# Optimization experiments

Measured on AMD Instinct MI355X. Metric: run time of the kernel, lower is better.

The kernel has to match this reference:

```python
import jax, jax.numpy as jnp
import numpy as np

B, L, DIM = 4, 2048, 512
H, D = 8, 64
SCALE = D ** -0.5
NEG = -10000.0


def setup_inputs() -> dict:
    key = jax.random.key(0)
    ks = jax.random.split(key, 5)
    std = 1.0 / np.sqrt(DIM)
    return {
        "x": jax.random.normal(ks[0], (B, L, DIM), dtype=jnp.float32),
        "wq": jax.random.normal(ks[1], (H * D, DIM), dtype=jnp.float32) * std,
        "wk": jax.random.normal(ks[2], (H * D, DIM), dtype=jnp.float32) * std,
        "wv": jax.random.normal(ks[3], (H * D, DIM), dtype=jnp.float32) * std,
        "wo": jax.random.normal(ks[4], (DIM, H * D), dtype=jnp.float32) * std,
    }


def reference(x, wq, wk, wv, wo):
    b, l, _ = x.shape
    # projections (torch Linear: y = x @ W.T), split heads -> [b,h,l,d]
    q = (x @ wq.T).reshape(b, l, H, D).transpose(0, 2, 1, 3)
    k = (x @ wk.T).reshape(b, l, H, D).transpose(0, 2, 1, 3)
    v = (x @ wv.T).reshape(b, l, H, D).transpose(0, 2, 1, 3)
    scores = jnp.einsum("bhld,bhsd->bhls", q, k) * SCALE
    scores = jnp.nan_to_num(scores, nan=0.0, posinf=10000.0, neginf=NEG)
    diag = jnp.eye(l, dtype=bool)[None, None]  # [1,1,l,l]
    scores = jnp.where(diag, NEG, scores)
    attn = jax.nn.softmax(scores, axis=-1)
    attn = jnp.where(diag, 0.0, attn)
    attn = jnp.nan_to_num(attn, nan=0.0, posinf=0.0, neginf=0.0)
    out = jnp.einsum("bhls,bhsd->bhld", attn, v)
    out = out.transpose(0, 2, 1, 3).reshape(b, l, H * D)
    return out @ wo.T
```

## Files before the change

### kernel.cpp

```cpp
#include <hip/hip_runtime.h>
#include <hip/hip_bf16.h>


#define Bsz 4
#define Lsz 2048
#define DIMsz 512
#define Hsz 8
#define Dsz 64

typedef _Float16 f16;
typedef __attribute__((ext_vector_type(8))) _Float16 f16x8;
typedef __attribute__((ext_vector_type(4))) _Float16 f16x4;
typedef __attribute__((ext_vector_type(2))) __fp16 fp16x2;
typedef __attribute__((ext_vector_type(4))) float f32x4;
typedef __attribute__((ext_vector_type(16))) float f32x16;
typedef unsigned int u32;
typedef __attribute__((ext_vector_type(2))) unsigned int u32x2;

#if __has_builtin(__builtin_amdgcn_exp2f)
#define EXP2(x) __builtin_amdgcn_exp2f(x)
#else
#define EXP2(x) __expf(0.6931471805599453f * (x))
#endif

__device__ __forceinline__ u32 pack2(float a, float b) {
#if __has_builtin(__builtin_amdgcn_cvt_pkrtz)
    fp16x2 h = __builtin_amdgcn_cvt_pkrtz(a, b);
    return __builtin_bit_cast(u32, h);
#else
    fp16x2 h; h.x = (__fp16)a; h.y = (__fp16)b;
    return __builtin_bit_cast(u32, h);
#endif
}

#if __has_builtin(__builtin_amdgcn_permlane32_swap)
__device__ __forceinline__ void plswap(u32& a, u32& b) {
    u32x2 r = __builtin_amdgcn_permlane32_swap(a, b, false, false);
    a = r.x; b = r.y;
}
#else
__device__ __forceinline__ void plswap(u32& a, u32& b) {
    u32 sa = (u32)__shfl_xor((int)a, 32);
    u32 sb = (u32)__shfl_xor((int)b, 32);
    bool hi = (threadIdx.x & 32) != 0;
    u32 na = hi ? sb : a;
    u32 nb = hi ? b : sa;
    a = na; b = nb;
}
#endif

__device__ __forceinline__ void gl2lds16(const void* g, void* l) {
    __builtin_amdgcn_global_load_lds(
        (const __attribute__((address_space(1))) u32*)g,
        (__attribute__((address_space(3))) u32*)l, 16, 0, 0);
}

__global__ __launch_bounds__(256) void pack_f16(
    const float* __restrict__ x, const float* __restrict__ wq,
    const float* __restrict__ wk, const float* __restrict__ wv,
    const float* __restrict__ wo,
    f16* __restrict__ xh, f16* __restrict__ w3h, f16* __restrict__ woh)
{
    int bx = blockIdx.x, seg, blk;
    if (bx < 4096) { seg = 0; blk = bx; }
    else { seg = 1 + ((bx - 4096) >> 8); blk = (bx - 4096) & 255; }
    const float* s; f16* d; float sc = 1.0f;
    switch (seg) {
        case 0: s = x;  d = xh;            break;
        case 1: s = wq; d = w3h;           sc = 0.18033688011112042f; break;
        case 2: s = wk; d = w3h + 262144;  break;
        case 3: s = wv; d = w3h + 524288;  break;
        default: s = wo; d = woh;          break;
    }
    int i = (blk * 256 + threadIdx.x) * 4;
    float4 v = *(const float4*)(s + i);
    f16x4 o;
    o.x = (f16)(v.x * sc); o.y = (f16)(v.y * sc);
    o.z = (f16)(v.z * sc); o.w = (f16)(v.w * sc);
    *(f16x4*)(d + i) = o;
}

__global__ __launch_bounds__(256) void gemm_qkv_f16(
    const f16* __restrict__ A, const f16* __restrict__ B,
    f16* __restrict__ qh, f16* __restrict__ kh, f16* __restrict__ vth)
{
    __shared__ __align__(16) char smem[32768];
    f16* Ash = (f16*)smem;
    f16* Bsh = (f16*)(smem + 16384);

    const int tid = threadIdx.x;
    const int w = tid >> 6, lane = tid & 63;
    const int quad = lane >> 4, low = lane & 15;
    const int wm = w >> 1, wn = w & 1;
    const int m0 = blockIdx.y * 128, n0 = blockIdx.x * 128;

    f32x4 acc[4][4];
    #pragma unroll
    for (int i = 0; i < 4; i++)
        #pragma unroll
        for (int j = 0; j < 4; j++) acc[i][j] = (f32x4){0.f, 0.f, 0.f, 0.f};

    #pragma unroll 1
    for (int k0 = 0; k0 < DIMsz; k0 += 64) {
        __syncthreads();
        #pragma unroll
        for (int j = 0; j < 4; j++) {
            int t = j * 256 + tid;
            int r = t >> 3, g = t & 7;
            int gc = (g ^ (r & 7)) * 8;
            char* lb = (char*)Ash + (j * 256 + w * 64) * 16;
            gl2lds16(A + (size_t)(m0 + r) * DIMsz + k0 + gc, lb);
            char* lb2 = (char*)Bsh + (j * 256 + w * 64) * 16;
            gl2lds16(B + (size_t)(n0 + r) * DIMsz + k0 + gc, lb2);
        }
        __syncthreads();

        #pragma unroll
        for (int ks2 = 0; ks2 < 2; ks2++) {
            f16x8 af[4], bf[4];
            #pragma unroll
            for (int mt = 0; mt < 4; mt++) {
                int ar = wm * 64 + mt * 16 + low;
                int c = ks2 * 4 + quad;
                af[mt] = *(const f16x8*)&Ash[ar * 64 + ((c ^ (ar & 7)) << 3)];
            }
            #pragma unroll
            for (int nt = 0; nt < 4; nt++) {
                int br = wn * 64 + nt * 16 + low;
                int c = ks2 * 4 + quad;
                bf[nt] = *(const f16x8*)&Bsh[br * 64 + ((c ^ (br & 7)) << 3)];
            }
            #pragma unroll
            for (int mt = 0; mt < 4; mt++)
                #pragma unroll
                for (int nt = 0; nt < 4; nt++)
                    acc[mt][nt] = __builtin_amdgcn_mfma_f32_16x16x32_f16(
                        af[mt], bf[nt], acc[mt][nt], 0, 0, 0);
        }
    }

    const int proj = n0 >> 9;
    if (proj < 2) {
        f16* dst = (proj == 0) ? qh : kh;
        #pragma unroll
        for (int nt = 0; nt < 4; nt++) {
            int n = n0 + wn * 64 + nt * 16 + low;
            int c = n & 511, h = c >> 6, d = c & 63;
            #pragma unroll
            for (int mt = 0; mt < 4; mt++)
                #pragma unroll
                for (int r = 0; r < 4; r++) {
                    int m = m0 + wm * 64 + mt * 16 + quad * 4 + r;
                    int b_ = m >> 11, l = m & (Lsz - 1);
                    size_t bh = (size_t)(b_ * Hsz + h);
                    dst[(bh * Lsz + l) * Dsz + d] = (f16)acc[mt][nt][r];
                }
        }
    } else {
        const int hb = (n0 & 511) >> 6;
        f16* Tv = (f16*)smem;
        const int b_ = m0 >> 11, l0 = m0 & (Lsz - 1);
        #pragma unroll 1
        for (int hs = 0; hs < 2; hs++) {
            __syncthreads();
            if (wn == hs) {
                #pragma unroll
                for (int nt = 0; nt < 4; nt++) {
                    int d = nt * 16 + low;
                    #pragma unroll
                    for (int mt = 0; mt < 4; mt++)
                        #pragma unroll
                        for (int r = 0; r < 4; r++) {
                            int l = wm * 64 + mt * 16 + quad * 4 + r;
                            Tv[d * 136 + l] = (f16)acc[mt][nt][r];
                        }
                }
            }
            __syncthreads();
            int d = tid >> 2, seg = tid & 3;
            size_t bh = (size_t)(b_ * Hsz + hb + hs);
            f16* dstp = vth + (bh * 64 + d) * (size_t)Lsz + l0 + seg * 32;
            const f16* srcp = Tv + d * 136 + seg * 32;
            #pragma unroll
            for (int j = 0; j < 4; j++)
                *(f16x8*)(dstp + j * 8) = *(const f16x8*)(srcp + j * 8);
        }
    }
}

__global__ __launch_bounds__(256) void attn_mfma(
    const f16* __restrict__ q, const f16* __restrict__ k,
    const f16* __restrict__ vt, f16* __restrict__ ctx)
{
    __shared__ __align__(16) char smem[32768];
    __shared__ float Ls[2][32];

    f16* Ks = (f16*)smem;
    f16* Vs = (f16*)(smem + 16384);

    const int tid = threadIdx.x;
    const int w = tid >> 6, lane = tid & 63;
    const int col = lane & 31;
    const int h = lane >> 5;
    const int bh = blockIdx.x;
    const int qb = blockIdx.y;
    const int grp = w >> 1;
    const int kw = w & 1;
    const int q0w = qb * 64 + grp * 32;
    const size_t kvb = (size_t)bh * Lsz;

    f16x8 qf[4];
    #pragma unroll
    for (int s = 0; s < 4; s++)
        qf[s] = *(const f16x8*)(q + (kvb + q0w + col) * Dsz + s * 16 + h * 8);

    f32x16 acc[2];
    #pragma unroll
    for (int dt = 0; dt < 2; dt++)
        #pragma unroll
        for (int i = 0; i < 16; i++) acc[dt][i] = 0.f;
    float lsum = 0.f;

    #pragma unroll 1
    for (int s0 = 0; s0 < Lsz; s0 += 128) {
        __syncthreads();
        #pragma unroll
        for (int i = 0; i < 4; i++) {
            int idx = i * 256 + tid;
            int rk = idx >> 3, gk = idx & 7;
            int rv = idx >> 4, gv = idx & 15;
            char* kl = (char*)Ks + (i * 256 + w * 64) * 16;
            char* vl = (char*)Vs + (i * 256 + w * 64) * 16;
            gl2lds16(k + (kvb + s0 + rk) * Dsz + ((gk ^ (rk & 7)) << 3), kl);
            gl2lds16(vt + ((size_t)bh * Dsz + rv) * Lsz + s0 + ((gv ^ (rv & 15)) << 3), vl);
        }
        __syncthreads();

        #pragma unroll
        for (int sc = 0; sc < 2; sc++) {
            f32x16 st;
            #pragma unroll
            for (int i = 0; i < 16; i++) st[i] = 0.f;
            const int rk = sc * 64 + kw * 32 + col;
            #pragma unroll
            for (int s = 0; s < 4; s++) {
                f16x8 kf = *(const f16x8*)(Ks + rk * 64 +
                               (((s * 2 + h) ^ (rk & 7)) << 3));
                st = __builtin_amdgcn_mfma_f32_32x32x16_f16(kf, qf[s], st, 0, 0, 0);
            }

            float pv[16];
            #pragma unroll
            for (int i = 0; i < 16; i++) pv[i] = EXP2(st[i]);
            if (s0 + sc * 64 == qb * 64 && kw == grp) {
                #pragma unroll
                for (int i = 0; i < 16; i++) {
                    int row = (i & 3) + 8 * (i >> 2) + 4 * h;
                    pv[i] = (row == col) ? 0.f : pv[i];
                }
            }
            #pragma unroll
            for (int i = 0; i < 16; i++) lsum += pv[i];

            u32 P2[8];
            #pragma unroll
            for (int j = 0; j < 8; j++)
                P2[j] = pack2(pv[2 * j], pv[2 * j + 1]);
            plswap(P2[0], P2[2]); plswap(P2[1], P2[3]);
            plswap(P2[4], P2[6]); plswap(P2[5], P2[7]);
            union { u32 u[4]; f16x8 v; } pf[2];
            #pragma unroll
            for (int jj = 0; jj < 4; jj++) { pf[0].u[jj] = P2[jj]; pf[1].u[jj] = P2[4 + jj]; }

            #pragma unroll
            for (int dt = 0; dt < 2; dt++) {
                const int rv = dt * 32 + col;
                #pragma unroll
                for (int ks = 0; ks < 2; ks++) {
                    int cv = sc * 8 + kw * 4 + ks * 2 + h;
                    f16x8 vf = *(const f16x8*)(Vs + rv * 128 +
                                   ((cv ^ (rv & 15)) << 3));
                    acc[dt] = __builtin_amdgcn_mfma_f32_32x32x16_f16(
                        vf, pf[ks].v, acc[dt], 0, 0, 0);
                }
            }
        }
    }

    lsum += __shfl_xor(lsum, 32);

    __syncthreads();
    float* Om = (float*)smem;
    if (kw == 1) {
        float* og = Om + grp * 64 * 32;
        #pragma unroll
        for (int dt = 0; dt < 2; dt++)
            #pragma unroll
            for (int i = 0; i < 16; i++) {
                int row = (i & 3) + 8 * (i >> 2) + 4 * h;
                og[(dt * 32 + row) * 32 + col] = acc[dt][i];
            }
        if (h == 0) Ls[grp][col] = lsum;
    }
    __syncthreads();
    if (kw == 0) {
        const float* og = Om + grp * 64 * 32;
        #pragma unroll
        for (int dt = 0; dt < 2; dt++)
            #pragma unroll
            for (int i = 0; i < 16; i++) {
                int row = (i & 3) + 8 * (i >> 2) + 4 * h;
                acc[dt][i] += og[(dt * 32 + row) * 32 + col];
            }
        lsum += Ls[grp][col];
        const float inv = 1.0f / lsum;

        const int b = bh >> 3, hh = bh & 7;
        f16* op = ctx + ((size_t)(b * Lsz + q0w + col)) * DIMsz + hh * 64;
        #pragma unroll
        for (int dt = 0; dt < 2; dt++)
            #pragma unroll
            for (int r4 = 0; r4 < 4; r4++) {
                f16x4 o;
                o.x = (f16)(acc[dt][4 * r4 + 0] * inv);
                o.y = (f16)(acc[dt][4 * r4 + 1] * inv);
                o.z = (f16)(acc[dt][4 * r4 + 2] * inv);
                o.w = (f16)(acc[dt][4 * r4 + 3] * inv);
                *(f16x4*)(op + dt * 32 + 8 * r4 + 4 * h) = o;
            }
    }
}

__global__ __launch_bounds__(256) void gemm_out_f16(
    const f16* __restrict__ A, const f16* __restrict__ B,
    float* __restrict__ C)
{
    __shared__ f16 Ash[64 * 64];
    __shared__ f16 Bsh[64 * 64];
    const int tid = threadIdx.x;
    const int w = tid >> 6, lane = tid & 63;
    const int quad = lane >> 4, low = lane & 15;
    const int wm = w >> 1, wn = w & 1;
    const int m0 = blockIdx.y * 64, n0 = blockIdx.x * 64;

    f32x4 acc[2][2];
    #pragma unroll
    for (int i = 0; i < 2; i++)
        #pragma unroll
        for (int j = 0; j < 2; j++) acc[i][j] = (f32x4){0.f, 0.f, 0.f, 0.f};

    #pragma unroll 1
    for (int k0 = 0; k0 < DIMsz; k0 += 64) {
        __syncthreads();
        #pragma unroll
        for (int j = 0; j < 2; j++) {
            int t = j * 256 + tid;
            int r = t >> 3, g = t & 7;
            int gc = (g ^ (r & 7)) * 8;
            char* lb = (char*)Ash + (j * 256 + w * 64) * 16;
            gl2lds16(A + (size_t)(m0 + r) * DIMsz + k0 + gc, lb);
            char* lb2 = (char*)Bsh + (j * 256 + w * 64) * 16;
            gl2lds16(B + (size_t)(n0 + r) * DIMsz + k0 + gc, lb2);
        }
        __syncthreads();

        #pragma unroll
        for (int ks2 = 0; ks2 < 2; ks2++) {
            f16x8 af[2], bf[2];
            #pragma unroll
            for (int mt = 0; mt < 2; mt++) {
                int ar = wm * 32 + mt * 16 + low;
                int c = ks2 * 4 + quad;
                af[mt] = *(const f16x8*)&Ash[ar * 64 + ((c ^ (ar & 7)) << 3)];
            }
            #pragma unroll
            for (int nt = 0; nt < 2; nt++) {
                int br = wn * 32 + nt * 16 + low;
                int c = ks2 * 4 + quad;
                bf[nt] = *(const f16x8*)&Bsh[br * 64 + ((c ^ (br & 7)) << 3)];
            }
            #pragma unroll
            for (int mt = 0; mt < 2; mt++)
                #pragma unroll
                for (int nt = 0; nt < 2; nt++)
                    acc[mt][nt] = __builtin_amdgcn_mfma_f32_16x16x32_f16(
                        af[mt], bf[nt], acc[mt][nt], 0, 0, 0);
        }
    }

    #pragma unroll
    for (int mt = 0; mt < 2; mt++)
        #pragma unroll
        for (int r = 0; r < 4; r++) {
            int m = m0 + wm * 32 + mt * 16 + quad * 4 + r;
            #pragma unroll
            for (int nt = 0; nt < 2; nt++) {
                int n = n0 + wn * 32 + nt * 16 + low;
                C[(size_t)m * DIMsz + n] = acc[mt][nt][r];
            }
        }
}

extern "C" void kernel_launch(void* const* d_in, const int* in_sizes, int n_in,
                              void* d_out, int out_size, void* d_ws, size_t ws_size,
                              hipStream_t stream) {
    const float* x  = (const float*)d_in[0];
    const float* wq = (const float*)d_in[1];
    const float* wk = (const float*)d_in[2];
    const float* wv = (const float*)d_in[3];
    const float* wo = (const float*)d_in[4];
    float* out = (float*)d_out;

    const size_t NTOK = (size_t)Bsz * Lsz;
    const size_t XSZ  = NTOK * DIMsz;

    f16* xh   = (f16*)d_ws;
    f16* w3h  = xh + XSZ;
    f16* woh  = w3h + 3 * 262144;
    f16* qh   = woh + 262144;
    f16* kh   = qh + XSZ;
    f16* vth  = kh + XSZ;
    f16* ctxh = vth + XSZ;

    pack_f16<<<5120, 256, 0, stream>>>(x, wq, wk, wv, wo, xh, w3h, woh);

    dim3 g1(1536 / 128, NTOK / 128);
    gemm_qkv_f16<<<g1, 256, 0, stream>>>(xh, w3h, qh, kh, vth);

    dim3 g2(Bsz * Hsz, Lsz / 64);
    attn_mfma<<<g2, 256, 0, stream>>>(qh, kh, vth, ctxh);

    dim3 g3(DIMsz / 64, NTOK / 64);
    gemm_out_f16<<<g3, 256, 0, stream>>>(ctxh, woh, out);
}
```

Measured before the change: 168.5 us.

## Restructure attention to 32-query blocks with direct K loads and 4-way key split

The attention kernel now has each block handle 32 queries with four waves splitting the keys, instead of 64 queries with pairs of waves. K fragments are read straight from global memory into registers rather than staged through LDS, and only V is staged, with half the shared memory and a launch bound of two blocks. The row sum is accumulated from packed fp16 pairs with a dot2 instruction, and partial outputs are reduced across the four waves through LDS. Separately, the output GEMM moves to a 128-wide K tile to halve its barrier count. The trade is more blocks and duplicate global K/V traffic, plus extra reduction barriers.

```diff
diff --git a/kernel.cpp b/kernel.cpp
--- a/kernel.cpp
+++ b/kernel.cpp
@@ -30,6 +30,16 @@
 #else
     fp16x2 h; h.x = (__fp16)a; h.y = (__fp16)b;
     return __builtin_bit_cast(u32, h);
+#endif
+}
+
+__device__ __forceinline__ float addpair(u32 p, float c) {
+#if __has_builtin(__builtin_amdgcn_fdot2)
+    fp16x2 ones; ones.x = (__fp16)1.0f; ones.y = (__fp16)1.0f;
+    return __builtin_amdgcn_fdot2(__builtin_bit_cast(fp16x2, p), ones, c, false);
+#else
+    fp16x2 h = __builtin_bit_cast(fp16x2, p);
+    return c + (float)h.x + (float)h.y;
 #endif
 }
 
@@ -188,15 +198,12 @@
     }
 }
 
-__global__ __launch_bounds__(256) void attn_mfma(
+__global__ __launch_bounds__(256, 2) void attn_mfma(
     const f16* __restrict__ q, const f16* __restrict__ k,
     const f16* __restrict__ vt, f16* __restrict__ ctx)
 {
-    __shared__ __align__(16) char smem[32768];
-    __shared__ float Ls[2][32];
-
-    f16* Ks = (f16*)smem;
-    f16* Vs = (f16*)(smem + 16384);
+    __shared__ __align__(16) char smem[16384];
+    __shared__ float Ls[4][32];
 
     const int tid = threadIdx.x;
     const int w = tid >> 6, lane = tid & 63;
@@ -204,15 +211,32 @@
     const int h = lane >> 5;
     const int bh = blockIdx.x;
     const int qb = blockIdx.y;
-    const int grp = w >> 1;
-    const int kw = w & 1;
-    const int q0w = qb * 64 + grp * 32;
+    const int q0 = qb * 32;
     const size_t kvb = (size_t)bh * Lsz;
 
     f16x8 qf[4];
     #pragma unroll
     for (int s = 0; s < 4; s++)
-        qf[s] = *(const f16x8*)(q + (kvb + q0w + col) * Dsz + s * 16 + h * 8);
+        qf[s] = *(const f16x8*)(q + (kvb + q0 + col) * Dsz + s * 16 + h * 8);
+
+    const f16* kgp = k + (kvb + w * 32 + col) * Dsz + h * 8;
+
+    const f16* vp;
+    {
+        int rv = tid >> 4, gv = tid & 15;
+        vp = vt + ((size_t)bh * Dsz + rv) * Lsz + ((gv ^ (rv & 15)) << 3);
+    }
+    f16* Vs = (f16*)smem;
+    char* vl = (char*)Vs + (w * 64) * 16;
+
+    const f16* vfp[2][2];
+    #pragma unroll
+    for (int dt = 0; dt < 2; dt++)
+        #pragma unroll
+        for (int ks = 0; ks < 2; ks++) {
+            int rv = dt * 32 + col, cv = w * 4 + ks * 2 + h;
+            vfp[dt][ks] = Vs + rv * 128 + ((cv ^ (rv & 15)) << 3);
+        }
 
     f32x16 acc[2];
     #pragma unroll
@@ -221,78 +245,72 @@
         for (int i = 0; i < 16; i++) acc[dt][i] = 0.f;
     float lsum = 0.f;
 
+    const int drnd_i = qb >> 2;
+    const int dw = qb & 3;
+
     #pragma unroll 1
-    for (int s0 = 0; s0 < Lsz; s0 += 128) {
-        __syncthreads();
-        #pragma unroll
-        for (int i = 0; i < 4; i++) {
-            int idx = i * 256 + tid;
-            int rk = idx >> 3, gk = idx & 7;
-            int rv = idx >> 4, gv = idx & 15;
-            char* kl = (char*)Ks + (i * 256 + w * 64) * 16;
-            char* vl = (char*)Vs + (i * 256 + w * 64) * 16;
-            gl2lds16(k + (kvb + s0 + rk) * Dsz + ((gk ^ (rk & 7)) << 3), kl);
-            gl2lds16(vt + ((size_t)bh * Dsz + rv) * Lsz + s0 + ((gv ^ (rv & 15)) << 3), vl);
-        }
-        __syncthreads();
-
-        #pragma unroll
-        for (int sc = 0; sc < 2; sc++) {
-            f32x16 st;
-            #pragma unroll
-            for (int i = 0; i < 16; i++) st[i] = 0.f;
-            const int rk = sc * 64 + kw * 32 + col;
-            #pragma unroll
-            for (int s = 0; s < 4; s++) {
-                f16x8 kf = *(const f16x8*)(Ks + rk * 64 +
-                               (((s * 2 + h) ^ (rk & 7)) << 3));
-                st = __builtin_amdgcn_mfma_f32_32x32x16_f16(kf, qf[s], st, 0, 0, 0);
-            }
-
-            float pv[16];
-            #pragma unroll
-            for (int i = 0; i < 16; i++) pv[i] = EXP2(st[i]);
-            if (s0 + sc * 64 == qb * 64 && kw == grp) {
-                #pragma unroll
-                for (int i = 0; i < 16; i++) {
-                    int row = (i & 3) + 8 * (i >> 2) + 4 * h;
-                    pv[i] = (row == col) ? 0.f : pv[i];
-                }
-            }
-            #pragma unroll
-            for (int i = 0; i < 16; i++) lsum += pv[i];
-
-            u32 P2[8];
-            #pragma unroll
-            for (int j = 0; j < 8; j++)
-                P2[j] = pack2(pv[2 * j], pv[2 * j + 1]);
-            plswap(P2[0], P2[2]); plswap(P2[1], P2[3]);
-            plswap(P2[4], P2[6]); plswap(P2[5], P2[7]);
-            union { u32 u[4]; f16x8 v; } pf[2];
-            #pragma unroll
-            for (int jj = 0; jj < 4; jj++) { pf[0].u[jj] = P2[jj]; pf[1].u[jj] = P2[4 + jj]; }
-
-            #pragma unroll
-            for (int dt = 0; dt < 2; dt++) {
-                const int rv = dt * 32 + col;
-                #pragma unroll
-                for (int ks = 0; ks < 2; ks++) {
-                    int cv = sc * 8 + kw * 4 + ks * 2 + h;
-                    f16x8 vf = *(const f16x8*)(Vs + rv * 128 +
-                                   ((cv ^ (rv & 15)) << 3));
-                    acc[dt] = __builtin_amdgcn_mfma_f32_32x32x16_f16(
-                        vf, pf[ks].v, acc[dt], 0, 0, 0);
-                }
-            }
-        }
+    for (int r = 0; r < 16; r++) {
+        __syncthreads();
+        gl2lds16(vp,            vl);
+        gl2lds16(vp + 16 * Lsz, vl + 4096);
+        gl2lds16(vp + 32 * Lsz, vl + 8192);
+        gl2lds16(vp + 48 * Lsz, vl + 12288);
+        vp += 128;
+
+        f16x8 kf[4];
+        #pragma unroll
+        for (int s = 0; s < 4; s++)
+            kf[s] = *(const f16x8*)(kgp + s * 16);
+        kgp += 128 * Dsz;
+
+        f32x16 st;
+        #pragma unroll
+        for (int i = 0; i < 16; i++) st[i] = 0.f;
+        #pragma unroll
+        for (int s = 0; s < 4; s++)
+            st = __builtin_amdgcn_mfma_f32_32x32x16_f16(kf[s], qf[s], st, 0, 0, 0);
+
+        float pv[16];
+        #pragma unroll
+        for (int i = 0; i < 16; i++) pv[i] = EXP2(st[i]);
+        if (r == drnd_i && w == dw) {
+            #pragma unroll
+            for (int i = 0; i < 16; i++) {
+                int row = (i & 3) + 8 * (i >> 2) + 4 * h;
+                pv[i] = (row == col) ? 0.f : pv[i];
+            }
+        }
+        u32 P2[8];
+        #pragma unroll
+        for (int j = 0; j < 8; j++) {
+            P2[j] = pack2(pv[2 * j], pv[2 * j + 1]);
+            lsum = addpair(P2[j], lsum);
+        }
+        plswap(P2[0], P2[2]); plswap(P2[1], P2[3]);
+        plswap(P2[4], P2[6]); plswap(P2[5], P2[7]);
+        union { u32 u[4]; f16x8 v; } pf[2];
+        #pragma unroll
+        for (int jj = 0; jj < 4; jj++) { pf[0].u[jj] = P2[jj]; pf[1].u[jj] = P2[4 + jj]; }
+
+        __syncthreads();
+
+        #pragma unroll
+        for (int dt = 0; dt < 2; dt++)
+            #pragma unroll
+            for (int ks = 0; ks < 2; ks++) {
+                f16x8 vf = *(const f16x8*)vfp[dt][ks];
+                acc[dt] = __builtin_amdgcn_mfma_f32_32x32x16_f16(
+                    vf, pf[ks].v, acc[dt], 0, 0, 0);
+            }
     }
 
     lsum += __shfl_xor(lsum, 32);
-
+    if (h == 0) Ls[w][col] = lsum;
+
+    float* Om = (float*)smem;
     __syncthreads();
-    float* Om = (float*)smem;
-    if (kw == 1) {
-        float* og = Om + grp * 64 * 32;
+    if (w & 1) {
+        float* og = Om + (w >> 1) * 2048;
         #pragma unroll
         for (int dt = 0; dt < 2; dt++)
             #pragma unroll
@@ -300,11 +318,10 @@
                 int row = (i & 3) + 8 * (i >> 2) + 4 * h;
                 og[(dt * 32 + row) * 32 + col] = acc[dt][i];
             }
-        if (h == 0) Ls[grp][col] = lsum;
     }
     __syncthreads();
-    if (kw == 0) {
-        const float* og = Om + grp * 64 * 32;
+    if (!(w & 1)) {
+        const float* og = Om + (w >> 1) * 2048;
         #pragma unroll
         for (int dt = 0; dt < 2; dt++)
             #pragma unroll
@@ -312,11 +329,30 @@
                 int row = (i & 3) + 8 * (i >> 2) + 4 * h;
                 acc[dt][i] += og[(dt * 32 + row) * 32 + col];
             }
-        lsum += Ls[grp][col];
-        const float inv = 1.0f / lsum;
-
-        const int b = bh >> 3, hh = bh & 7;
-        f16* op = ctx + ((size_t)(b * Lsz + q0w + col)) * DIMsz + hh * 64;
+    }
+    __syncthreads();
+    if (w == 2) {
+        #pragma unroll
+        for (int dt = 0; dt < 2; dt++)
+            #pragma unroll
+            for (int i = 0; i < 16; i++) {
+                int row = (i & 3) + 8 * (i >> 2) + 4 * h;
+                Om[(dt * 32 + row) * 32 + col] = acc[dt][i];
+            }
+    }
+    __syncthreads();
+    if (w == 0) {
+        #pragma unroll
+        for (int dt = 0; dt < 2; dt++)
+            #pragma unroll
+            for (int i = 0; i < 16; i++) {
+                int row = (i & 3) + 8 * (i >> 2) + 4 * h;
+                acc[dt][i] += Om[(dt * 32 + row) * 32 + col];
+            }
+        float ls = Ls[0][col] + Ls[1][col] + Ls[2][col] + Ls[3][col];
+        const float inv = 1.0f / ls;
+        const int bb = bh >> 3, hh = bh & 7;
+        f16* op = ctx + ((size_t)(bb * Lsz + q0 + col)) * DIMsz + hh * 64;
         #pragma unroll
         for (int dt = 0; dt < 2; dt++)
             #pragma unroll
@@ -335,8 +371,8 @@
     const f16* __restrict__ A, const f16* __restrict__ B,
     float* __restrict__ C)
 {
-    __shared__ f16 Ash[64 * 64];
-    __shared__ f16 Bsh[64 * 64];
+    __shared__ f16 Ash[64 * 128];
+    __shared__ f16 Bsh[64 * 128];
     const int tid = threadIdx.x;
     const int w = tid >> 6, lane = tid & 63;
     const int quad = lane >> 4, low = lane & 15;
@@ -350,13 +386,13 @@
         for (int j = 0; j < 2; j++) acc[i][j] = (f32x4){0.f, 0.f, 0.f, 0.f};
 
     #pragma unroll 1
-    for (int k0 = 0; k0 < DIMsz; k0 += 64) {
-        __syncthreads();
-        #pragma unroll
-        for (int j = 0; j < 2; j++) {
+    for (int k0 = 0; k0 < DIMsz; k0 += 128) {
+        __syncthreads();
+        #pragma unroll
+        for (int j = 0; j < 4; j++) {
             int t = j * 256 + tid;
-            int r = t >> 3, g = t & 7;
-            int gc = (g ^ (r & 7)) * 8;
+            int r = t >> 4, g = t & 15;
+            int gc = (g ^ (r & 15)) * 8;
             char* lb = (char*)Ash + (j * 256 + w * 64) * 16;
             gl2lds16(A + (size_t)(m0 + r) * DIMsz + k0 + gc, lb);
             char* lb2 = (char*)Bsh + (j * 256 + w * 64) * 16;
@@ -365,19 +401,19 @@
         __syncthreads();
 
         #pragma unroll
-        for (int ks2 = 0; ks2 < 2; ks2++) {
+        for (int ks2 = 0; ks2 < 4; ks2++) {
             f16x8 af[2], bf[2];
             #pragma unroll
             for (int mt = 0; mt < 2; mt++) {
                 int ar = wm * 32 + mt * 16 + low;
                 int c = ks2 * 4 + quad;
-                af[mt] = *(const f16x8*)&Ash[ar * 64 + ((c ^ (ar & 7)) << 3)];
+                af[mt] = *(const f16x8*)&Ash[ar * 128 + ((c ^ (ar & 15)) << 3)];
             }
             #pragma unroll
             for (int nt = 0; nt < 2; nt++) {
                 int br = wn * 32 + nt * 16 + low;
                 int c = ks2 * 4 + quad;
-                bf[nt] = *(const f16x8*)&Bsh[br * 64 + ((c ^ (br & 7)) << 3)];
+                bf[nt] = *(const f16x8*)&Bsh[br * 128 + ((c ^ (br & 15)) << 3)];
             }
             #pragma unroll
             for (int mt = 0; mt < 2; mt++)
@@ -427,7 +463,7 @@
     dim3 g1(1536 / 128, NTOK / 128);
     gemm_qkv_f16<<<g1, 256, 0, stream>>>(xh, w3h, qh, kh, vth);
 
-    dim3 g2(Bsz * Hsz, Lsz / 64);
+    dim3 g2(Bsz * Hsz, Lsz / 32);
     attn_mfma<<<g2, 256, 0, stream>>>(qh, kh, vth, ctxh);
 
     dim3 g3(DIMsz / 64, NTOK / 64);
```

New measurement: 198.2 us. 17.6% more time.
